# Performance work log

Hardware: AMD Instinct MI355X
Metric: run time of the kernel (lower is better)

Reference implementation:

```python
import jax, jax.numpy as jnp
import numpy as np

N_TRAIN, DIM, OUT_DIM, BATCH = 16384, 64, 8, 8192


def setup_inputs() -> dict:
    key = jax.random.key(0)
    k1, k2, k3 = jax.random.split(key, 3)
    batches = jax.random.uniform(k1, (BATCH, DIM), dtype=jnp.float32)
    x_training = jax.random.uniform(k2, (N_TRAIN, DIM), dtype=jnp.float32)
    y_training = jax.random.normal(k3, (N_TRAIN, OUT_DIM), dtype=jnp.float32)
    beta = jnp.ones((1, N_TRAIN), dtype=jnp.float32) / 0.1  # matches ones/0.1 init
    return {"batches": batches, "x_training": x_training,
            "y_training": y_training, "beta": beta}


def reference(batches, x_training, y_training, beta):
    # Pairwise Euclidean distances [batch, n_train] via the expanded form
    # (avoids the O(batch*n_train*dim) repeated tensor the torch code builds).
    b2 = jnp.sum(batches * batches, axis=1, keepdims=True)        # [B, 1]
    x2 = jnp.sum(x_training * x_training, axis=1)[None, :]        # [1, N]
    sq = jnp.maximum(b2 + x2 - 2.0 * (batches @ x_training.T), 0.0)
    dist = jnp.sqrt(sq)                                           # [B, N]
    radial_val = jnp.exp(-beta * dist)                            # RBF kernel [B, N]
    psum1 = jnp.sum(radial_val, axis=1, keepdims=True)            # [B, 1]
    psum2 = radial_val @ y_training                               # [B, OUT_DIM]
    return psum2 / psum1
```

## Files before the change

### kernel.cpp

```cpp
#include <hip/hip_runtime.h>
#include <math.h>
#include <stdint.h>

#define NTRAIN 16384
#define DIM 64
#define ODIM 8
#define BATCH 8192
#define LOG2E 1.4426950408889634f

typedef float f32x4 __attribute__((ext_vector_type(4)));
typedef _Float16 f16x8 __attribute__((ext_vector_type(8)));
typedef short short8 __attribute__((ext_vector_type(8)));
typedef unsigned short u16;

static __device__ __forceinline__ u16 f2h(float f) {
  return __builtin_bit_cast(u16, (_Float16)f);
}
static __device__ __forceinline__ float h2f(u16 h) {
  return (float)__builtin_bit_cast(_Float16, h);
}
static __device__ __forceinline__ u16 f2bf(float f) {
  unsigned u = __builtin_bit_cast(unsigned, f);
  u += 0x7FFFu + ((u >> 16) & 1u);
  return (u16)(u >> 16);
}

static __device__ __forceinline__ f32x4 mfma_h32(f16x8 a, f16x8 b, f32x4 c) {
  return __builtin_amdgcn_mfma_f32_16x16x32_f16(a, b, c, 0, 0, 0);
}
static __device__ __forceinline__ f32x4 mfma_bf32(short8 a, short8 b, f32x4 c) {
  return __builtin_amdgcn_mfma_f32_16x16x32_bf16(a, b, c, 0, 0, 0);
}
static __device__ __forceinline__ float ex2n(float x) {
  float r;
  asm("v_exp_f32 %0, -%1" : "=v"(r) : "v"(x));
  return r;
}
static __device__ __forceinline__ unsigned pkbf(float a, float b) {
  unsigned d;
  asm("v_cvt_pk_bf16_f32 %0, %1, %2" : "=v"(d) : "v"(a), "v"(b));
  return d;
}

__global__ __launch_bounds__(256) void k_frag(
    const float* __restrict__ xt, const float* __restrict__ yt,
    const float* __restrict__ beta,
    u16* __restrict__ xf, u16* __restrict__ yv) {
  int tid = blockIdx.x * 256 + threadIdx.x;

  if (tid < (NTRAIN / 16) * 64) {
    int tile = tid >> 6, lane = tid & 63;
    int lr = lane & 15, lg = lane >> 4;
    int n = tile * 16 + lr;
    float g = beta[n] * LOG2E;
    float g2v = g * g;
    float s2g = 2.0f * g2v;
    const float* row = xt + (size_t)n * DIM;
    float4 a0 = *(const float4*)(row + lg * 8);
    float4 a1 = *(const float4*)(row + lg * 8 + 4);
    float4 b0 = *(const float4*)(row + 32 + lg * 8);
    float4 b1 = *(const float4*)(row + 32 + lg * 8 + 4);
    float ssq = 0.f;
    ssq = fmaf(a0.x, a0.x, ssq); ssq = fmaf(a0.y, a0.y, ssq);
    ssq = fmaf(a0.z, a0.z, ssq); ssq = fmaf(a0.w, a0.w, ssq);
    ssq = fmaf(a1.x, a1.x, ssq); ssq = fmaf(a1.y, a1.y, ssq);
    ssq = fmaf(a1.z, a1.z, ssq); ssq = fmaf(a1.w, a1.w, ssq);
    ssq = fmaf(b0.x, b0.x, ssq); ssq = fmaf(b0.y, b0.y, ssq);
    ssq = fmaf(b0.z, b0.z, ssq); ssq = fmaf(b0.w, b0.w, ssq);
    ssq = fmaf(b1.x, b1.x, ssq); ssq = fmaf(b1.y, b1.y, ssq);
    ssq = fmaf(b1.z, b1.z, ssq); ssq = fmaf(b1.w, b1.w, ssq);
    ssq += __shfl_xor(ssq, 16);
    ssq += __shfl_xor(ssq, 32);

    uint4 u0, u1;
    {
      unsigned e[8];
      float v[8] = {a0.x, a0.y, a0.z, a0.w, a1.x, a1.y, a1.z, a1.w};
#pragma unroll
      for (int j = 0; j < 8; ++j) e[j] = f2h(s2g * v[j]);
      u0.x = e[0] | (e[1] << 16); u0.y = e[2] | (e[3] << 16);
      u0.z = e[4] | (e[5] << 16); u0.w = e[6] | (e[7] << 16);
    }
    {
      unsigned e[8];
      float v[8] = {b0.x, b0.y, b0.z, b0.w, b1.x, b1.y, b1.z, b1.w};
#pragma unroll
      for (int j = 0; j < 8; ++j) e[j] = f2h(s2g * v[j]);
      u1.x = e[0] | (e[1] << 16); u1.y = e[2] | (e[3] << 16);
      u1.z = e[4] | (e[5] << 16); u1.w = e[6] | (e[7] << 16);
    }
    uint4 u2 = {0, 0, 0, 0};
    if (lg == 0) {
      float gx2v = g2v * ssq;
      u16 xh = f2h(gx2v);
      u16 xl = f2h(gx2v - h2f(xh));
      u16 gh = f2h(g2v);
      u16 gl = f2h(g2v - h2f(gh));
      u2.x = (unsigned)xh | ((unsigned)xl << 16);
      u2.y = (unsigned)gh | ((unsigned)gh << 16);
      u2.z = (unsigned)gl;
    }
    uint4* dst = (uint4*)xf + (size_t)tile * 3 * 64;
    dst[0 * 64 + lane] = u0;
    dst[1 * 64 + lane] = u1;
    dst[2 * 64 + lane] = u2;
    return;
  }
  tid -= (NTRAIN / 16) * 64;

  if (tid < (NTRAIN / 32) * 64) {
    int t = tid >> 6, lane = tid & 63;
    int col = lane & 15, lg = lane >> 4;
    unsigned e[8];
#pragma unroll
    for (int j = 0; j < 8; ++j) {
      int n = t * 32 + ((j < 4) ? (lg * 4 + j) : (16 + lg * 4 + (j - 4)));
      float v = (col == 0) ? 1.0f
                           : ((col < 9) ? yt[(size_t)n * ODIM + (col - 1)] : 0.0f);
      e[j] = f2bf(v);
    }
    uint4 u;
    u.x = e[0] | (e[1] << 16); u.y = e[2] | (e[3] << 16);
    u.z = e[4] | (e[5] << 16); u.w = e[6] | (e[7] << 16);
    ((uint4*)yv)[(size_t)t * 64 + lane] = u;
  }
}

#define LOADX3(X_, nbv)                                                       \
  {                                                                           \
    const size_t fb_ = (size_t)((nbv) >> 4) * 3;                              \
    X_[0] = xf4[(fb_ + 0) * 64 + lane];                                       \
    X_[1] = xf4[(fb_ + 1) * 64 + lane];                                       \
    X_[2] = xf4[(fb_ + 2) * 64 + lane];                                       \
  }

#define SCOMP(X_, t_, U0_, U1_)                                               \
  {                                                                           \
    f32x4 sA = {0.f, 0.f, 0.f, 0.f};                                          \
    __builtin_amdgcn_s_setprio(1);                                            \
    sA = mfma_h32(__builtin_bit_cast(f16x8, X_[2]), BN[t_], sA);              \
    sA = mfma_h32(__builtin_bit_cast(f16x8, X_[0]), BH[t_][0], sA);           \
    sA = mfma_h32(__builtin_bit_cast(f16x8, X_[1]), BH[t_][1], sA);           \
    __builtin_amdgcn_s_setprio(0);                                            \
    float w0 = ex2n(__builtin_amdgcn_sqrtf(fabsf(sA[0])));                    \
    float w1 = ex2n(__builtin_amdgcn_sqrtf(fabsf(sA[1])));                    \
    float w2 = ex2n(__builtin_amdgcn_sqrtf(fabsf(sA[2])));                    \
    float w3 = ex2n(__builtin_amdgcn_sqrtf(fabsf(sA[3])));                    \
    U0_ = pkbf(w0, w1);                                                       \
    U1_ = pkbf(w2, w3);                                                       \
  }

__global__ __launch_bounds__(256, 4) void grnn_pass1(
    const u16* __restrict__ xf, const u16* __restrict__ yv,
    const float* __restrict__ batches,
    float* __restrict__ partial, int chunk_n, int nc) {
  const int lane = threadIdx.x & 63;
  const int lr = lane & 15, lg = lane >> 4;

  int mt, c;
  if (nc == 32) {
    const int bid = blockIdx.x;
    const int xcd = bid & 7;
    const int q = bid >> 3;
    c = xcd + 8 * (q & 3);
    mt = q >> 2;
  } else {
    mt = blockIdx.x % (BATCH / 256);
    c = blockIdx.x / (BATCH / 256);
  }
  const int mbase = mt * 256 + (threadIdx.x >> 6) * 64;
  const int n0 = c * chunk_n;
  const int npair = chunk_n / 32;

  f16x8 BH[4][2], BN[4];
  f32x4 pv[4];
#pragma unroll
  for (int t = 0; t < 4; ++t) {
    const int mrow = mbase + t * 16 + lr;
    float ssum = 0.f;
#pragma unroll
    for (int ks = 0; ks < 2; ++ks) {
      const float* src = batches + (size_t)mrow * DIM + ks * 32 + lg * 8;
      float4 v0 = *(const float4*)src;
      float4 v1 = *(const float4*)(src + 4);
      BH[t][ks][0] = (_Float16)v0.x; BH[t][ks][1] = (_Float16)v0.y;
      BH[t][ks][2] = (_Float16)v0.z; BH[t][ks][3] = (_Float16)v0.w;
      BH[t][ks][4] = (_Float16)v1.x; BH[t][ks][5] = (_Float16)v1.y;
      BH[t][ks][6] = (_Float16)v1.z; BH[t][ks][7] = (_Float16)v1.w;
      ssum = fmaf(v0.x, v0.x, ssum); ssum = fmaf(v0.y, v0.y, ssum);
      ssum = fmaf(v0.z, v0.z, ssum); ssum = fmaf(v0.w, v0.w, ssum);
      ssum = fmaf(v1.x, v1.x, ssum); ssum = fmaf(v1.y, v1.y, ssum);
      ssum = fmaf(v1.z, v1.z, ssum); ssum = fmaf(v1.w, v1.w, ssum);
    }
    ssum += __shfl_xor(ssum, 16);
    ssum += __shfl_xor(ssum, 32);
#pragma unroll
    for (int j = 0; j < 8; ++j) BN[t][j] = (_Float16)0.0f;
    if (lg == 0) {
      _Float16 bh = (_Float16)ssum;
      _Float16 bl = (_Float16)(ssum - (float)bh);
      BN[t][0] = (_Float16)(-1.0f);
      BN[t][1] = (_Float16)(-1.0f);
      BN[t][2] = -bh;
      BN[t][3] = -bl;
      BN[t][4] = -bh;
    }
    pv[t] = (f32x4){0.f, 0.f, 0.f, 0.f};
  }

  const uint4* xf4 = (const uint4*)xf;
  const uint4* yv4 = (const uint4*)yv;

  uint4 Xa[3], Xb[3], Vp, Vn;
  LOADX3(Xa, n0)
  LOADX3(Xb, n0 + 16)
  Vp = yv4[(size_t)(n0 >> 5) * 64 + lane];

  for (int p = 0; p < npair; ++p) {
    const int nb = n0 + p * 32;
    unsigned A0[4], A1[4], B0[4], B1[4];
#pragma unroll
    for (int t = 0; t < 4; ++t) SCOMP(Xa, t, A0[t], A1[t])
    if (p + 1 < npair) LOADX3(Xa, nb + 32)
#pragma unroll
    for (int t = 0; t < 4; ++t) SCOMP(Xb, t, B0[t], B1[t])
    if (p + 1 < npair) {
      LOADX3(Xb, nb + 48)
      Vn = yv4[(size_t)((nb + 32) >> 5) * 64 + lane];
    }
#pragma unroll
    for (int t = 0; t < 4; ++t) {
      uint4 pa = {A0[t], A1[t], B0[t], B1[t]};
      pv[t] = mfma_bf32(__builtin_bit_cast(short8, pa),
                        __builtin_bit_cast(short8, Vp), pv[t]);
    }
    Vp = Vn;
  }

  float* pc = partial + (size_t)c * 9 * BATCH;
  if (lr < 9) {
#pragma unroll
    for (int t = 0; t < 4; ++t)
#pragma unroll
      for (int r = 0; r < 4; ++r)
        pc[(size_t)lr * BATCH + (mbase + t * 16 + lg * 4 + r)] = pv[t][r];
  }
}

__global__ __launch_bounds__(64) void grnn_pass2(const float* __restrict__ partial,
                                                 float* __restrict__ out, int nc) {
  const int lane = threadIdx.x & 63;
  const int half = lane >> 5;
  const int b = blockIdx.x * 32 + (lane & 31);
  const int per = nc >> 1;

  float s[9];
#pragma unroll
  for (int j = 0; j < 9; ++j) s[j] = 0.f;
  for (int cc = half * per; cc < half * per + per; ++cc) {
    const float* p = partial + (size_t)cc * 9 * BATCH;
#pragma unroll
    for (int j = 0; j < 9; ++j) s[j] += p[(size_t)j * BATCH + b];
  }
  if ((nc & 1) && half == 0) {
    const float* p = partial + (size_t)(nc - 1) * 9 * BATCH;
#pragma unroll
    for (int j = 0; j < 9; ++j) s[j] += p[(size_t)j * BATCH + b];
  }
#pragma unroll
  for (int j = 0; j < 9; ++j) s[j] += __shfl_xor(s[j], 32);

  if (half == 0) {
    const float inv = 1.f / s[0];
#pragma unroll
    for (int j = 0; j < ODIM; ++j) out[(size_t)b * ODIM + j] = s[j + 1] * inv;
  }
}

extern "C" void kernel_launch(void* const* d_in, const int* in_sizes, int n_in,
                              void* d_out, int out_size, void* d_ws, size_t ws_size,
                              hipStream_t stream) {
  const float* batches = (const float*)d_in[0];
  const float* xt      = (const float*)d_in[1];
  const float* yt      = (const float*)d_in[2];
  const float* beta    = (const float*)d_in[3];
  float* out = (float*)d_out;

  const size_t xf_b = (size_t)(NTRAIN / 16) * 3 * 1024;
  const size_t yv_b = (size_t)(NTRAIN / 32) * 64 * 16;
  const size_t fixed = xf_b + yv_b;
  const size_t per_chunk = (size_t)9 * BATCH * 4;

  int nc = 32;
  while (nc > 1 && fixed + (size_t)nc * per_chunk > ws_size) nc >>= 1;
  const int chunk_n = NTRAIN / nc;

  char* p = (char*)d_ws;
  u16* xf = (u16*)p;      p += xf_b;
  u16* yv = (u16*)p;      p += yv_b;
  float* partial = (float*)p;

  const int frag_threads = (NTRAIN / 16) * 64 + (NTRAIN / 32) * 64;
  k_frag<<<(frag_threads + 255) / 256, 256, 0, stream>>>(xt, yt, beta, xf, yv);
  grnn_pass1<<<(BATCH / 256) * nc, 256, 0, stream>>>(
      xf, yv, batches, partial, chunk_n, nc);
  grnn_pass2<<<BATCH / 32, 64, 0, stream>>>(partial, out, nc);
}
```

Measured before the change: 66.72 us.

## Fuse final reduction into pass1 via last-block atomic counter and drop setprio

Removes the separate pass2 kernel launch. Each pass1 block atomically increments a per-batch-tile counter, and the last block to finish for that tile sums all chunk partials and writes the normalized output. The counters are zeroed in k_frag. It also drops the s_setprio hints around the MFMA sequence. The change saves a kernel launch and its dependency gap, but concentrates the final reduction on 32 blocks, which may tail-serialize.

```diff
diff --git a/kernel.cpp b/kernel.cpp
--- a/kernel.cpp
+++ b/kernel.cpp
@@ -45,8 +45,9 @@
 __global__ __launch_bounds__(256) void k_frag(
     const float* __restrict__ xt, const float* __restrict__ yt,
     const float* __restrict__ beta,
-    u16* __restrict__ xf, u16* __restrict__ yv) {
+    u16* __restrict__ xf, u16* __restrict__ yv, int* __restrict__ flags) {
   int tid = blockIdx.x * 256 + threadIdx.x;
+  if (tid < 64) flags[tid] = 0;
 
   if (tid < (NTRAIN / 16) * 64) {
     int tile = tid >> 6, lane = tid & 63;
@@ -137,11 +138,9 @@
 #define SCOMP(X_, t_, U0_, U1_)                                               \
   {                                                                           \
     f32x4 sA = {0.f, 0.f, 0.f, 0.f};                                          \
-    __builtin_amdgcn_s_setprio(1);                                            \
     sA = mfma_h32(__builtin_bit_cast(f16x8, X_[2]), BN[t_], sA);              \
     sA = mfma_h32(__builtin_bit_cast(f16x8, X_[0]), BH[t_][0], sA);           \
     sA = mfma_h32(__builtin_bit_cast(f16x8, X_[1]), BH[t_][1], sA);           \
-    __builtin_amdgcn_s_setprio(0);                                            \
     float w0 = ex2n(__builtin_amdgcn_sqrtf(fabsf(sA[0])));                    \
     float w1 = ex2n(__builtin_amdgcn_sqrtf(fabsf(sA[1])));                    \
     float w2 = ex2n(__builtin_amdgcn_sqrtf(fabsf(sA[2])));                    \
@@ -153,7 +152,9 @@
 __global__ __launch_bounds__(256, 4) void grnn_pass1(
     const u16* __restrict__ xf, const u16* __restrict__ yv,
     const float* __restrict__ batches,
-    float* __restrict__ partial, int chunk_n, int nc) {
+    float* __restrict__ partial, int* __restrict__ flags,
+    float* __restrict__ out, int chunk_n, int nc) {
+  __shared__ int is_last;
   const int lane = threadIdx.x & 63;
   const int lr = lane & 15, lg = lane >> 4;
 
@@ -245,32 +246,24 @@
       for (int r = 0; r < 4; ++r)
         pc[(size_t)lr * BATCH + (mbase + t * 16 + lg * 4 + r)] = pv[t][r];
   }
-}
-
-__global__ __launch_bounds__(64) void grnn_pass2(const float* __restrict__ partial,
-                                                 float* __restrict__ out, int nc) {
-  const int lane = threadIdx.x & 63;
-  const int half = lane >> 5;
-  const int b = blockIdx.x * 32 + (lane & 31);
-  const int per = nc >> 1;
-
-  float s[9];
-#pragma unroll
-  for (int j = 0; j < 9; ++j) s[j] = 0.f;
-  for (int cc = half * per; cc < half * per + per; ++cc) {
-    const float* p = partial + (size_t)cc * 9 * BATCH;
-#pragma unroll
-    for (int j = 0; j < 9; ++j) s[j] += p[(size_t)j * BATCH + b];
-  }
-  if ((nc & 1) && half == 0) {
-    const float* p = partial + (size_t)(nc - 1) * 9 * BATCH;
-#pragma unroll
-    for (int j = 0; j < 9; ++j) s[j] += p[(size_t)j * BATCH + b];
-  }
-#pragma unroll
-  for (int j = 0; j < 9; ++j) s[j] += __shfl_xor(s[j], 32);
-
-  if (half == 0) {
+
+  __threadfence();
+  if (threadIdx.x == 0) {
+    int old = atomicAdd(&flags[mt], 1);
+    is_last = (old == nc - 1) ? 1 : 0;
+  }
+  __syncthreads();
+  if (is_last) {
+    __threadfence();
+    const int b = mt * 256 + threadIdx.x;
+    float s[9];
+#pragma unroll
+    for (int j = 0; j < 9; ++j) s[j] = 0.f;
+    for (int cc = 0; cc < nc; ++cc) {
+      const float* p = partial + (size_t)cc * 9 * BATCH;
+#pragma unroll
+      for (int j = 0; j < 9; ++j) s[j] += p[(size_t)j * BATCH + b];
+    }
     const float inv = 1.f / s[0];
 #pragma unroll
     for (int j = 0; j < ODIM; ++j) out[(size_t)b * ODIM + j] = s[j + 1] * inv;
@@ -288,7 +281,8 @@
 
   const size_t xf_b = (size_t)(NTRAIN / 16) * 3 * 1024;
   const size_t yv_b = (size_t)(NTRAIN / 32) * 64 * 16;
-  const size_t fixed = xf_b + yv_b;
+  const size_t fl_b = 64 * sizeof(int);
+  const size_t fixed = xf_b + yv_b + fl_b;
   const size_t per_chunk = (size_t)9 * BATCH * 4;
 
   int nc = 32;
@@ -298,11 +292,12 @@
   char* p = (char*)d_ws;
   u16* xf = (u16*)p;      p += xf_b;
   u16* yv = (u16*)p;      p += yv_b;
+  int* flags = (int*)p;   p += fl_b;
   float* partial = (float*)p;
 
   const int frag_threads = (NTRAIN / 16) * 64 + (NTRAIN / 32) * 64;
-  k_frag<<<(frag_threads + 255) / 256, 256, 0, stream>>>(xt, yt, beta, xf, yv);
+  k_frag<<<(frag_threads + 255) / 256, 256, 0, stream>>>(
+      xt, yt, beta, xf, yv, flags);
   grnn_pass1<<<(BATCH / 256) * nc, 256, 0, stream>>>(
-      xf, yv, batches, partial, chunk_n, nc);
-  grnn_pass2<<<BATCH / 32, 64, 0, stream>>>(partial, out, nc);
-}
+      xf, yv, batches, partial, flags, out, chunk_n, nc);
+}
```

After: 194.9 us. +192.1%, slower.
